# Kernel optimization log

Measured on AMD Instinct MI355X. Metric: run time of the kernel, lower is better.

The kernel has to match this reference:

```python
import jax, jax.numpy as jnp
import numpy as np

B, N, F_IN, E, TOPK = 64, 1024, 64, 128, 32
NEG_SLOPE = 0.2  # GAT leaky-relu slope


def setup_inputs() -> dict:
    key = jax.random.key(0)
    ks = jax.random.split(key, 7)
    x = jax.random.normal(ks[0], (B, N, F_IN), dtype=jnp.float32)
    emb = jax.random.normal(ks[1], (N, E), dtype=jnp.float32)            # nn.Embedding table
    W_fe = jax.random.normal(ks[2], (F_IN, E), dtype=jnp.float32) / np.sqrt(F_IN).astype(np.float32)
    a_src = jax.random.normal(ks[3], (2 * E,), dtype=jnp.float32) * 0.05
    a_dst = jax.random.normal(ks[4], (2 * E,), dtype=jnp.float32) * 0.05
    lin_W = jax.random.normal(ks[5], (E, 1), dtype=jnp.float32) / np.sqrt(E).astype(np.float32)
    lin_b = jnp.zeros((1,), dtype=jnp.float32)
    return {"x": x, "emb": emb, "W_fe": W_fe, "a_src": a_src, "a_dst": a_dst,
            "lin_W": lin_W, "lin_b": lin_b}


def reference(x, emb, W_fe, a_src, a_dst, lin_W, lin_b):
    b, n, _ = x.shape
    e_dim = emb.shape[-1]
    # --- cosine-similarity topk graph construction (shared across batch) ---
    norm = jnp.linalg.norm(emb, axis=-1, keepdims=True)                  # [N,1]
    sim = (emb @ emb.T) / (norm @ norm.T)                                # [N,N]
    idx = jax.lax.top_k(sim, TOPK)[1]                                    # [N,K] int32 neighbor (target) nodes
    # --- graph attention feature extraction ---
    h = jnp.einsum('bnf,fe->bne', x, W_fe)                               # [B,N,E] projected node features
    g = jnp.concatenate([h, jnp.broadcast_to(emb, (b, n, e_dim))], -1)   # [B,N,2E] feat || embedding
    e_s = g @ a_src                                                      # [B,N] source attention term
    e_d = g @ a_dst                                                      # [B,N] target attention term
    # edges: source i repeated TOPK times -> targets idx[i]; softmax over each node's K neighbors
    scores = jax.nn.leaky_relu(e_s[:, :, None] + e_d[:, idx], NEG_SLOPE)  # [B,N,K]
    alpha = jax.nn.softmax(scores, axis=-1)                              # [B,N,K]
    h_dst = h[:, idx, :]                                                 # [B,N,K,E] gathered neighbor feats
    out = jnp.einsum('bnk,bnke->bne', alpha, h_dst)                      # aggregate messages
    out = jax.nn.relu(out)
    # --- linear readout ---
    y = out @ lin_W + lin_b                                              # [B,N,1]
    return y[..., 0]                                                     # [B,N]
```

## Files before the change

### kernel.cpp

```cpp
#include <hip/hip_runtime.h>
#include <math.h>

#define BB 64
#define NN 1024
#define F_IN 64
#define EE 128
#define TOPK 32
#define NEG_SLOPE 0.2f

typedef unsigned int uint;
typedef unsigned short ushort;
typedef unsigned long long ull;
typedef __attribute__((ext_vector_type(8))) short short8;
typedef __attribute__((ext_vector_type(4))) float f32x4;
typedef __attribute__((ext_vector_type(2))) float f32x2;

static __device__ __forceinline__ uint f2bf(float f) {
  const uint x = __float_as_uint(f);
  return (x + 0x7fffu + ((x >> 16) & 1u)) >> 16;
}
static __device__ __forceinline__ float bf_lo(uint u) {
  return __uint_as_float(u << 16);
}
static __device__ __forceinline__ float bf_hi_raw(uint u) {
  return __uint_as_float(u);
}
static __device__ __forceinline__ uint fmono(float f) {
  uint u = __float_as_uint(f);
  return (u & 0x80000000u) ? ~u : (u | 0x80000000u);
}
static __device__ __forceinline__ ull umax64(ull a, ull b) {
  return a > b ? a : b;
}
static __device__ __forceinline__ ull umin64(ull a, ull b) {
  return a < b ? a : b;
}
static __device__ __forceinline__ ull shfl_xor64(ull v, int mask) {
  const uint lo = __shfl_xor((uint)v, mask);
  const uint hi = __shfl_xor((uint)(v >> 32), mask);
  return ((ull)hi << 32) | lo;
}

__global__ __launch_bounds__(256) void k2a_sim(
    const float* __restrict__ emb, const float* __restrict__ a_src,
    const float* __restrict__ a_dst, const float* __restrict__ W_fe,
    uint* __restrict__ keys, float* __restrict__ u_src,
    float* __restrict__ u_dst, ushort* __restrict__ wt,
    float* __restrict__ rn) {
  __shared__ __align__(16) uint eni[16 * 64];
  __shared__ __align__(16) uint enj[256 * 64];
  const int t = threadIdx.x, wid = t >> 6, lane = t & 63;
  const int it = blockIdx.x >> 2, js = blockIdx.x & 3;
  const int i0 = it * 16, jw0 = js * 256;

  const int rh = t >> 1, h = t & 1;
#pragma unroll
  for (int p = 0; p < 2; ++p) {
    const int r = p * 128 + rh;
    const float* src = emb + (size_t)(jw0 + r) * EE + h * 64;
    float4 v[16];
#pragma unroll
    for (int q = 0; q < 16; ++q) v[q] = *(const float4*)&src[q * 4];
    float sq = 0.f;
#pragma unroll
    for (int q = 0; q < 16; ++q)
      sq += v[q].x * v[q].x + v[q].y * v[q].y + v[q].z * v[q].z +
            v[q].w * v[q].w;
    sq += __shfl_xor(sq, 1);
    const float rs = rsqrtf(sq);
    if (it == 0 && h == 0) rn[jw0 + r] = rs;
    char* dst = (char*)(enj + r * 64);
    const int swz = (r & 7) << 4;
#pragma unroll
    for (int s16 = 0; s16 < 8; ++s16) {
      const float4 a = v[s16 * 2], b2 = v[s16 * 2 + 1];
      uint4 w4;
      w4.x = f2bf(a.x * rs) | (f2bf(a.y * rs) << 16);
      w4.y = f2bf(a.z * rs) | (f2bf(a.w * rs) << 16);
      w4.z = f2bf(b2.x * rs) | (f2bf(b2.y * rs) << 16);
      w4.w = f2bf(b2.z * rs) | (f2bf(b2.w * rs) << 16);
      *(uint4*)(dst + ((h * 128 + s16 * 16) ^ swz)) = w4;
    }
  }
  if (t < 32) {
    const int r = t >> 1, hh = t & 1;
    const float* src = emb + (size_t)(i0 + r) * EE + hh * 64;
    float4 v[16];
#pragma unroll
    for (int q = 0; q < 16; ++q) v[q] = *(const float4*)&src[q * 4];
    float sq = 0.f;
#pragma unroll
    for (int q = 0; q < 16; ++q)
      sq += v[q].x * v[q].x + v[q].y * v[q].y + v[q].z * v[q].z +
            v[q].w * v[q].w;
    sq += __shfl_xor(sq, 1);
    const float rs = rsqrtf(sq);
    char* dst = (char*)(eni + r * 64);
    const int swz = (r & 7) << 4;
#pragma unroll
    for (int s16 = 0; s16 < 8; ++s16) {
      const float4 a = v[s16 * 2], b2 = v[s16 * 2 + 1];
      uint4 w4;
      w4.x = f2bf(a.x * rs) | (f2bf(a.y * rs) << 16);
      w4.y = f2bf(a.z * rs) | (f2bf(a.w * rs) << 16);
      w4.z = f2bf(b2.x * rs) | (f2bf(b2.y * rs) << 16);
      w4.w = f2bf(b2.z * rs) | (f2bf(b2.w * rs) << 16);
      *(uint4*)(dst + ((hh * 128 + s16 * 16) ^ swz)) = w4;
    }
  }
  __syncthreads();

  const int nn = lane & 15, quad = lane >> 4;
  short8 af[4];
#pragma unroll
  for (int s = 0; s < 4; ++s) {
    const int kb = (s * 64 + quad * 16) ^ ((nn & 7) << 4);
    af[s] = *(const short8*)((const char*)eni + nn * 256 + kb);
  }
  f32x4 acc[4];
#pragma unroll
  for (int t4 = 0; t4 < 4; ++t4) acc[t4] = (f32x4){0.f, 0.f, 0.f, 0.f};
#pragma unroll
  for (int t4 = 0; t4 < 4; ++t4) {
    const int rloc = wid * 64 + t4 * 16 + nn;
    const char* brow = (const char*)enj + rloc * 256;
    const int swz = (rloc & 7) << 4;
#pragma unroll
    for (int s = 0; s < 4; ++s) {
      const short8 bf = *(const short8*)(brow + ((s * 64 + quad * 16) ^ swz));
      acc[t4] =
          __builtin_amdgcn_mfma_f32_16x16x32_bf16(af[s], bf, acc[t4], 0, 0, 0);
    }
  }
#pragma unroll
  for (int t4 = 0; t4 < 4; ++t4) {
    const int j = jw0 + wid * 64 + t4 * 16 + nn;
#pragma unroll
    for (int reg = 0; reg < 4; ++reg) {
      const int i = i0 + quad * 4 + reg;
      keys[(size_t)i * NN + j] = fmono(acc[t4][reg]);
    }
  }

  if (js == 0) {
#pragma unroll
    for (int rr = 0; rr < 4; ++rr) {
      const int row = i0 + wid * 4 + rr;
      const float* er = emb + (size_t)row * EE;
      const float e0 = er[lane], e1 = er[64 + lane];
      float us = e0 * a_src[EE + lane] + e1 * a_src[EE + 64 + lane];
      float ud = e0 * a_dst[EE + lane] + e1 * a_dst[EE + 64 + lane];
#pragma unroll
      for (int o = 1; o <= 32; o <<= 1) {
        us += __shfl_xor(us, o);
        ud += __shfl_xor(ud, o);
      }
      if (lane == 0) {
        u_src[row] = us;
        u_dst[row] = ud;
      }
    }
  } else if (js == 1 && it < 32) {
    const int g = it * 256 + t;
    const int n = g >> 6, k = g & 63;
    wt[g] = (ushort)f2bf(W_fe[k * EE + n]);
  }
}

__global__ __launch_bounds__(256) void k23(
    const uint* __restrict__ keys, int* __restrict__ idx_out,
    const float* __restrict__ x, const ushort* __restrict__ wt,
    const float* __restrict__ a_src, const float* __restrict__ a_dst,
    const float* __restrict__ u_src, const float* __restrict__ u_dst,
    uint* __restrict__ h2, float* __restrict__ es, float* __restrict__ ed,
    const float* __restrict__ emb, const float* __restrict__ rn,
    float* __restrict__ y, const float* __restrict__ lin_b) {
  __shared__ ull cand[256];
  __shared__ float rowbuf[EE];
  const int t = threadIdx.x, wid = t >> 6, lane = t & 63;

  if (blockIdx.x < NN) {
    const int row = blockIdx.x;
    if (t < EE) rowbuf[t] = emb[(size_t)row * EE + t];

    const int jb = wid * 256 + lane * 4;
    const uint4 kv = *(const uint4*)&keys[(size_t)row * NN + jb];
    ull xr[4];
    xr[0] = ((ull)kv.x << 32) | (uint)(jb + 0);
    xr[1] = ((ull)kv.y << 32) | (uint)(jb + 1);
    xr[2] = ((ull)kv.z << 32) | (uint)(jb + 2);
    xr[3] = ((ull)kv.w << 32) | (uint)(jb + 3);

#pragma unroll
    for (int k = 2; k <= 256; k <<= 1) {
#pragma unroll
      for (int d = 128; d >= 1; d >>= 1) {
        if (d > (k >> 1)) continue;
        if (d >= 4) {
          const int pl = d >> 2;
          const bool lower = (lane & pl) == 0;
#pragma unroll
          for (int r = 0; r < 4; ++r) {
            const ull o = shfl_xor64(xr[r], pl);
            const bool desc = (((lane * 4 + r) & k) == 0);
            const bool keepmax = (desc == lower);
            xr[r] = keepmax ? umax64(xr[r], o) : umin64(xr[r], o);
          }
        } else if (d == 2) {
#pragma unroll
          for (int r = 0; r < 2; ++r) {
            const bool desc = (((lane * 4 + r) & k) == 0);
            const ull hi = umax64(xr[r], xr[r + 2]);
            const ull lo = umin64(xr[r], xr[r + 2]);
            xr[r] = desc ? hi : lo;
            xr[r + 2] = desc ? lo : hi;
          }
        } else {
#pragma unroll
          for (int r = 0; r < 4; r += 2) {
            const bool desc = (((lane * 4 + r) & k) == 0);
            const ull hi = umax64(xr[r], xr[r + 1]);
            const ull lo = umin64(xr[r], xr[r + 1]);
            xr[r] = desc ? hi : lo;
            xr[r + 1] = desc ? lo : hi;
          }
        }
      }
    }
    if (lane < 16) {
#pragma unroll
      for (int r = 0; r < 4; ++r) cand[wid * 64 + lane * 4 + r] = xr[r];
    }
    __syncthreads();

    if (wid < 2) {
      const ull a0 = cand[(2 * wid) * 64 + lane];
      const ull a1 = cand[(2 * wid) * 64 + 64 + 63 - lane];
      ull v0 = umax64(a0, a1);
#pragma unroll
      for (int d = 32; d >= 1; d >>= 1) {
        const ull o = shfl_xor64(v0, d);
        v0 = ((lane & d) == 0) ? umax64(v0, o) : umin64(v0, o);
      }
      cand[wid * 128 + lane] = v0;
    }
    __syncthreads();

    if (wid == 0) {
      const ull a0 = cand[lane];
      const ull a1 = cand[128 + 63 - lane];
      ull v0 = umax64(a0, a1);
#pragma unroll
      for (int d = 32; d >= 1; d >>= 1) {
        const ull o = shfl_xor64(v0, d);
        v0 = ((lane & d) == 0) ? umax64(v0, o) : umin64(v0, o);
      }
      cand[192 + lane] = v0 & 1023u;
    }
    __syncthreads();

    const int c = t >> 2, dq = t & 3;
    const int jc = (int)(uint)cand[192 + c];
    const float* ej = emb + (size_t)jc * EE + dq * 32;
    const float* rb = rowbuf + dq * 32;
    float dot = 0.f;
#pragma unroll
    for (int q = 0; q < 8; ++q) {
      const float4 a = *(const float4*)&ej[q * 4];
      const float4 b = *(const float4*)&rb[q * 4];
      dot += a.x * b.x + a.y * b.y + a.z * b.z + a.w * b.w;
    }
    dot += __shfl_xor(dot, 1);
    dot += __shfl_xor(dot, 2);
    if (dq == 0) {
      const float cosv = dot * rn[row] * rn[jc];
      cand[c] = ((ull)fmono(cosv) << 32) | (uint)jc;
    }
    __syncthreads();

    if (wid == 0) {
      ull v = cand[lane];
#pragma unroll
      for (int k = 2; k <= 64; k <<= 1) {
#pragma unroll
        for (int d0 = 32; d0 >= 1; d0 >>= 1) {
          if (d0 > (k >> 1)) continue;
          const ull o = shfl_xor64(v, d0);
          const bool up = (lane & k) == 0;
          v = (up == ((lane & d0) == 0)) ? umax64(v, o) : umin64(v, o);
        }
      }
      if (lane < 32) idx_out[(size_t)row * TOPK + lane] = (int)(v & 1023u);
    }
  } else {
    const int row0 = (blockIdx.x - NN) * 64;
    const int nn = lane & 15, quad = lane >> 4;
    const int row0w = row0 + wid * 16;

    short8 af[2];
#pragma unroll
    for (int s = 0; s < 2; ++s) {
      const float* xr2 = x + (size_t)(row0w + nn) * F_IN + s * 32 + quad * 8;
      const float4 v0 = *(const float4*)&xr2[0];
      const float4 v1 = *(const float4*)&xr2[4];
      af[s][0] = (short)f2bf(v0.x);
      af[s][1] = (short)f2bf(v0.y);
      af[s][2] = (short)f2bf(v0.z);
      af[s][3] = (short)f2bf(v0.w);
      af[s][4] = (short)f2bf(v1.x);
      af[s][5] = (short)f2bf(v1.y);
      af[s][6] = (short)f2bf(v1.z);
      af[s][7] = (short)f2bf(v1.w);
    }

    f32x4 acc[8];
#pragma unroll
    for (int T = 0; T < 8; ++T) acc[T] = (f32x4){0.f, 0.f, 0.f, 0.f};

#pragma unroll
    for (int T = 0; T < 8; ++T) {
#pragma unroll
      for (int s = 0; s < 2; ++s) {
        const short8 bf =
            *(const short8*)&wt[(T * 16 + nn) * F_IN + s * 32 + quad * 8];
        acc[T] =
            __builtin_amdgcn_mfma_f32_16x16x32_bf16(af[s], bf, acc[T], 0, 0, 0);
      }
    }

    const int growbase = row0w + quad * 4;
#pragma unroll
    for (int reg = 0; reg < 4; ++reg) {
      uint* hr = h2 + (size_t)(growbase + reg) * 64 + nn;
#pragma unroll
      for (int T4 = 0; T4 < 4; ++T4) {
        hr[T4 * 16] =
            f2bf(acc[2 * T4][reg]) | (f2bf(acc[2 * T4 + 1][reg]) << 16);
      }
    }
    float ae[8], de[8];
#pragma unroll
    for (int T = 0; T < 8; ++T) {
      ae[T] = a_src[T * 16 + nn];
      de[T] = a_dst[T * 16 + nn];
    }
    const float bias = lin_b[0];
#pragma unroll
    for (int reg = 0; reg < 4; ++reg) {
      float ps = 0.f, pd = 0.f;
#pragma unroll
      for (int T = 0; T < 8; ++T) {
        ps += acc[T][reg] * ae[T];
        pd += acc[T][reg] * de[T];
      }
#pragma unroll
      for (int o = 1; o <= 8; o <<= 1) {
        ps += __shfl_xor(ps, o);
        pd += __shfl_xor(pd, o);
      }
      if (nn == 0) {
        const int grow = growbase + reg;
        const int node = grow & (NN - 1);
        es[grow] = ps + u_src[node];
        ed[grow] = pd + u_dst[node];
        y[grow] = bias;
      }
    }
  }
}

#define JV(K)                                             \
  (((K) & 3) == 0   ? jv[(K) >> 2].x                      \
   : ((K) & 3) == 1 ? jv[(K) >> 2].y                      \
   : ((K) & 3) == 2 ? jv[(K) >> 2].z                      \
                    : jv[(K) >> 2].w)

__global__ __launch_bounds__(256, 1) void k4_attn(
    const uint* __restrict__ h2, const float* __restrict__ es,
    const float* __restrict__ ed, const int* __restrict__ idx,
    const float* __restrict__ lin_W, const float* __restrict__ lin_b,
    float* __restrict__ y) {
  __shared__ __align__(16) uint hs[NN * 32];
  const int t = threadIdx.x, wid = t >> 6, lane = t & 63;
  const int o = lane >> 3, sub = lane & 7;
  const int g = blockIdx.x;
  const int q = (g & 7) * 16 + (g >> 4);
  const int nh = (g >> 3) & 1;
  const int b = q >> 1, dh = q & 1;

  const uint* hb = h2 + (size_t)b * NN * 64;
  const float* edb = ed + (size_t)b * NN;
  const float* esb = es + (size_t)b * NN;

#pragma unroll
  for (int i = 0; i < 32; ++i) {
    const int j = wid * 256 + i * 8 + o;
    const uint4 v = *(const uint4*)(hb + (size_t)j * 64 + dh * 32 + sub * 4);
    *(uint4*)(hs + j * 32 + sub * 4) = v;
  }
  __syncthreads();

  float lwlo[4], lwhi[4];
#pragma unroll
  for (int i = 0; i < 4; ++i) {
    const int u = dh * 32 + sub * 4 + i;
    const int T4 = u >> 4, nn2 = u & 15;
    lwlo[i] = lin_W[T4 * 32 + nn2];
    lwhi[i] = lin_W[T4 * 32 + 16 + nn2];
  }

  for (int it = 0; it < 16; ++it) {
    const int n = nh * 512 + wid * 128 + it * 8 + o;
    const int* ir = idx + n * TOPK;
    int4 jv[8];
#pragma unroll
    for (int qq = 0; qq < 8; ++qq) jv[qq] = *(const int4*)(ir + qq * 4);

    float4 tv[32];
#pragma unroll
    for (int k = 0; k < 32; ++k)
      tv[k] = *(const float4*)(hs + JV(k) * 32 + sub * 4);
    __builtin_amdgcn_sched_barrier(0);

    const float esv = esb[n];
    float p[32];
    float dsum = 0.f;
#pragma unroll
    for (int k = 0; k < 32; ++k) {
      float s = esv + edb[JV(k)];
      s = s > 0.f ? s : NEG_SLOPE * s;
      p[k] = __expf(s);
      dsum += p[k];
    }
    const float rs = 1.0f / dsum;

    f32x2 accA = {0.f, 0.f}, accB = {0.f, 0.f};
    f32x2 accC = {0.f, 0.f}, accD = {0.f, 0.f};
#pragma unroll
    for (int k = 0; k < 32; ++k) {
      const float wk = p[k] * rs;
      const float4 u = tv[k];
      f32x2 wp;
      wp.x = wk;
      wp.y = wk;
      f32x2 hi01, hi23, lo01, lo23;
      hi01.x = u.x;
      hi01.y = u.y;
      hi23.x = u.z;
      hi23.y = u.w;
      lo01.x = bf_lo(__float_as_uint(u.x));
      lo01.y = bf_lo(__float_as_uint(u.y));
      lo23.x = bf_lo(__float_as_uint(u.z));
      lo23.y = bf_lo(__float_as_uint(u.w));
      asm("v_pk_fma_f32 %0, %1, %2, %0" : "+v"(accA) : "v"(lo01), "v"(wp));
      asm("v_pk_fma_f32 %0, %1, %2, %0" : "+v"(accB) : "v"(hi01), "v"(wp));
      asm("v_pk_fma_f32 %0, %1, %2, %0" : "+v"(accC) : "v"(lo23), "v"(wp));
      asm("v_pk_fma_f32 %0, %1, %2, %0" : "+v"(accD) : "v"(hi23), "v"(wp));
    }

    float r = fmaxf(accA.x, 0.f) * lwlo[0] + fmaxf(accA.y, 0.f) * lwlo[1] +
              fmaxf(accB.x, 0.f) * lwhi[0] + fmaxf(accB.y, 0.f) * lwhi[1] +
              fmaxf(accC.x, 0.f) * lwlo[2] + fmaxf(accC.y, 0.f) * lwlo[3] +
              fmaxf(accD.x, 0.f) * lwhi[2] + fmaxf(accD.y, 0.f) * lwhi[3];
    r += __shfl_xor(r, 1);
    r += __shfl_xor(r, 2);
    r += __shfl_xor(r, 4);
    if (sub == 0) atomicAdd(&y[(size_t)b * NN + n], r);
  }
}

extern "C" void kernel_launch(void* const* d_in, const int* in_sizes, int n_in,
                              void* d_out, int out_size, void* d_ws,
                              size_t ws_size, hipStream_t stream) {
  const float* x = (const float*)d_in[0];
  const float* emb = (const float*)d_in[1];
  const float* W_fe = (const float*)d_in[2];
  const float* a_src = (const float*)d_in[3];
  const float* a_dst = (const float*)d_in[4];
  const float* lin_W = (const float*)d_in[5];
  const float* lin_b = (const float*)d_in[6];
  float* y = (float*)d_out;

  char* ws = (char*)d_ws;
  float* rn = (float*)(ws + 0);
  float* u_src = (float*)(ws + 4096);
  float* u_dst = (float*)(ws + 8192);
  int* idx = (int*)(ws + 16384);
  float* es = (float*)(ws + 147456);
  float* ed = (float*)(ws + 409600);
  uint* h2 = (uint*)(ws + 671744);
  uint* keys = (uint*)(ws + 17448960);
  ushort* wt = (ushort*)(ws + 21643264);

  k2a_sim<<<256, 256, 0, stream>>>(emb, a_src, a_dst, W_fe, keys, u_src,
                                   u_dst, wt, rn);
  k23<<<2048, 256, 0, stream>>>(keys, idx, x, wt, a_src, a_dst, u_src, u_dst,
                                h2, es, ed, emb, rn, y, lin_b);
  k4_attn<<<256, 256, 0, stream>>>(h2, es, ed, idx, lin_W, lin_b, y);
}
```

Before: 149.7 us.

## Precompute quantized softmax weights in separate kernel and pad LDS rows

Splits the softmax weight computation out of the attention kernel into a new kernel that writes the 32 per-node weights as 16-bit fixed-point values, reusing the keys workspace buffer. The aggregation kernel now runs 512-thread blocks, pads shared-memory rows from 32 to 36 words to reduce bank conflicts, and remaps blocks so each XCD handles a contiguous set of batches. The aim is to remove the exp and gather work from the gather-heavy inner loop and raise occupancy. In exchange it adds an extra launch and global round trip, and the weights are quantized to 16 bits, which costs precision.

After: 135.2 us. 1.11x faster.

```diff
diff --git a/kernel.cpp b/kernel.cpp
--- a/kernel.cpp
+++ b/kernel.cpp
@@ -375,28 +375,70 @@
    : ((K) & 3) == 2 ? jv[(K) >> 2].z                      \
                     : jv[(K) >> 2].w)
 
-__global__ __launch_bounds__(256, 1) void k4_attn(
-    const uint* __restrict__ h2, const float* __restrict__ es,
-    const float* __restrict__ ed, const int* __restrict__ idx,
-    const float* __restrict__ lin_W, const float* __restrict__ lin_b,
+__global__ __launch_bounds__(256) void kw(
+    const float* __restrict__ es, const float* __restrict__ ed,
+    const int* __restrict__ idx, uint* __restrict__ w16) {
+  const int t = threadIdx.x, blk = blockIdx.x;
+  const int b = blk >> 2;
+  const int n = (blk & 3) * 256 + t;
+  const int bn = b * NN + n;
+  const float esv = es[bn];
+  const float* edb = ed + (size_t)b * NN;
+  const int* ir = idx + n * TOPK;
+  int4 jv[8];
+#pragma unroll
+  for (int qq = 0; qq < 8; ++qq) jv[qq] = *(const int4*)(ir + qq * 4);
+  float p[32];
+  float dsum = 0.f;
+#pragma unroll
+  for (int k = 0; k < 32; ++k) {
+    float s = esv + edb[JV(k)];
+    s = s > 0.f ? s : NEG_SLOPE * s;
+    p[k] = __expf(s);
+    dsum += p[k];
+  }
+  const float sc = 65535.0f / dsum;
+  uint4 o4[4];
+  uint* op = (uint*)o4;
+#pragma unroll
+  for (int i = 0; i < 16; ++i) {
+    const uint a = (uint)(p[2 * i] * sc + 0.5f);
+    const uint bq = (uint)(p[2 * i + 1] * sc + 0.5f);
+    op[i] = a | (bq << 16);
+  }
+  uint4* dst = (uint4*)(w16 + (size_t)bn * 16);
+#pragma unroll
+  for (int i = 0; i < 4; ++i) dst[i] = o4[i];
+}
+
+#define WU(K)                                          \
+  ((((K) >> 1) & 3) == 0   ? wv[(K) >> 3].x            \
+   : (((K) >> 1) & 3) == 1 ? wv[(K) >> 3].y            \
+   : (((K) >> 1) & 3) == 2 ? wv[(K) >> 3].z            \
+                           : wv[(K) >> 3].w)
+#define WC(K) (((K) & 1) ? (WU(K) >> 16) : (WU(K) & 0xffffu))
+
+__global__ __launch_bounds__(512, 2) void k4_attn(
+    const uint* __restrict__ h2, const int* __restrict__ idx,
+    const uint* __restrict__ w16, const float* __restrict__ lin_W,
     float* __restrict__ y) {
-  __shared__ __align__(16) uint hs[NN * 32];
-  const int t = threadIdx.x, wid = t >> 6, lane = t & 63;
+  __shared__ __align__(16) uint hs[NN * 36];
+  const int t = threadIdx.x;
+  const int wid = t >> 6, lane = t & 63;
   const int o = lane >> 3, sub = lane & 7;
   const int g = blockIdx.x;
-  const int q = (g & 7) * 16 + (g >> 4);
-  const int nh = (g >> 3) & 1;
-  const int b = q >> 1, dh = q & 1;
-
-  const uint* hb = h2 + (size_t)b * NN * 64;
-  const float* edb = ed + (size_t)b * NN;
-  const float* esb = es + (size_t)b * NN;
-
-#pragma unroll
-  for (int i = 0; i < 32; ++i) {
-    const int j = wid * 256 + i * 8 + o;
-    const uint4 v = *(const uint4*)(hb + (size_t)j * 64 + dh * 32 + sub * 4);
-    *(uint4*)(hs + j * 32 + sub * 4) = v;
+  const int xcd = g & 7, r = g >> 3;
+  const int lb = r >> 2, dh = (r >> 1) & 1, nh = r & 1;
+  const int b = xcd * 8 + lb;
+
+  const uint* hb = h2 + (size_t)b * NN * 64 + dh * 32;
+
+#pragma unroll
+  for (int i = 0; i < 16; ++i) {
+    const int li = i * 512 + t;
+    const int j = li >> 3, s8 = li & 7;
+    const uint4 v = *(const uint4*)(hb + (size_t)j * 64 + s8 * 4);
+    *(uint4*)(hs + j * 36 + s8 * 4) = v;
   }
   __syncthreads();
 
@@ -409,8 +451,8 @@
     lwhi[i] = lin_W[T4 * 32 + 16 + nn2];
   }
 
-  for (int it = 0; it < 16; ++it) {
-    const int n = nh * 512 + wid * 128 + it * 8 + o;
+  for (int it = 0; it < 8; ++it) {
+    const int n = nh * 512 + wid * 64 + it * 8 + o;
     const int* ir = idx + n * TOPK;
     int4 jv[8];
 #pragma unroll
@@ -419,26 +461,18 @@
     float4 tv[32];
 #pragma unroll
     for (int k = 0; k < 32; ++k)
-      tv[k] = *(const float4*)(hs + JV(k) * 32 + sub * 4);
+      tv[k] = *(const float4*)(hs + (JV(k) * 36 + sub * 4));
+    uint4 wv[4];
+#pragma unroll
+    for (int i = 0; i < 4; ++i)
+      wv[i] = *(const uint4*)(w16 + (size_t)(b * NN + n) * 16 + i * 4);
     __builtin_amdgcn_sched_barrier(0);
-
-    const float esv = esb[n];
-    float p[32];
-    float dsum = 0.f;
-#pragma unroll
-    for (int k = 0; k < 32; ++k) {
-      float s = esv + edb[JV(k)];
-      s = s > 0.f ? s : NEG_SLOPE * s;
-      p[k] = __expf(s);
-      dsum += p[k];
-    }
-    const float rs = 1.0f / dsum;
 
     f32x2 accA = {0.f, 0.f}, accB = {0.f, 0.f};
     f32x2 accC = {0.f, 0.f}, accD = {0.f, 0.f};
 #pragma unroll
     for (int k = 0; k < 32; ++k) {
-      const float wk = p[k] * rs;
+      const float wk = (float)WC(k);
       const float4 u = tv[k];
       f32x2 wp;
       wp.x = wk;
@@ -458,14 +492,15 @@
       asm("v_pk_fma_f32 %0, %1, %2, %0" : "+v"(accD) : "v"(hi23), "v"(wp));
     }
 
-    float r = fmaxf(accA.x, 0.f) * lwlo[0] + fmaxf(accA.y, 0.f) * lwlo[1] +
-              fmaxf(accB.x, 0.f) * lwhi[0] + fmaxf(accB.y, 0.f) * lwhi[1] +
-              fmaxf(accC.x, 0.f) * lwlo[2] + fmaxf(accC.y, 0.f) * lwlo[3] +
-              fmaxf(accD.x, 0.f) * lwhi[2] + fmaxf(accD.y, 0.f) * lwhi[3];
-    r += __shfl_xor(r, 1);
-    r += __shfl_xor(r, 2);
-    r += __shfl_xor(r, 4);
-    if (sub == 0) atomicAdd(&y[(size_t)b * NN + n], r);
+    float r2 = fmaxf(accA.x, 0.f) * lwlo[0] + fmaxf(accA.y, 0.f) * lwlo[1] +
+               fmaxf(accB.x, 0.f) * lwhi[0] + fmaxf(accB.y, 0.f) * lwhi[1] +
+               fmaxf(accC.x, 0.f) * lwlo[2] + fmaxf(accC.y, 0.f) * lwlo[3] +
+               fmaxf(accD.x, 0.f) * lwhi[2] + fmaxf(accD.y, 0.f) * lwhi[3];
+    r2 *= 1.5259021897e-05f;
+    r2 += __shfl_xor(r2, 1);
+    r2 += __shfl_xor(r2, 2);
+    r2 += __shfl_xor(r2, 4);
+    if (sub == 0) atomicAdd(&y[(size_t)b * NN + n], r2);
   }
 }
 
@@ -491,10 +526,12 @@
   uint* h2 = (uint*)(ws + 671744);
   uint* keys = (uint*)(ws + 17448960);
   ushort* wt = (ushort*)(ws + 21643264);
+  uint* w16 = keys;
 
   k2a_sim<<<256, 256, 0, stream>>>(emb, a_src, a_dst, W_fe, keys, u_src,
                                    u_dst, wt, rn);
   k23<<<2048, 256, 0, stream>>>(keys, idx, x, wt, a_src, a_dst, u_src, u_dst,
                                 h2, es, ed, emb, rn, y, lin_b);
-  k4_attn<<<256, 256, 0, stream>>>(h2, es, ed, idx, lin_W, lin_b, y);
-}
+  kw<<<256, 256, 0, stream>>>(es, ed, idx, w16);
+  k4_attn<<<256, 512, 0, stream>>>(h2, idx, w16, lin_W, y);
+}
```
